# Kernel optimization log

Measured on AMD Instinct MI355X. Metric: run time of the kernel, lower is better.

The kernel has to match this reference:

```python
import jax, jax.numpy as jnp
import numpy as np

# Model dims (match init_kwargs)
D_MODEL = 1024
D_INNER = 2048
D_STATE = 16
D_CONV = 4
DT_RANK = 64
H = 8                      # num_heads
P = D_INNER // H           # head_dim = 256
DT_MIN, DT_MAX = 1e-4, 1.0
BATCH, SEQ = 2, 4096
TOTAL_OUT = 2 * D_INNER + DT_RANK + 2 * H * D_STATE  # 4416 (no gated delta)
EPS = 1e-6


def _xavier(k, shape):
    fan_out, fan_in = shape
    return jax.random.normal(k, shape, jnp.float32) * np.sqrt(2.0 / (fan_in + fan_out))


def setup_inputs() -> dict:
    key = jax.random.key(0)
    ks = jax.random.split(key, 8)
    x = jax.random.normal(ks[0], (BATCH, SEQ, D_MODEL), jnp.float32)
    W_in = _xavier(ks[1], (TOTAL_OUT, D_MODEL))          # in_proj (no bias)
    W_dt = _xavier(ks[2], (H, DT_RANK))                  # dt_proj (no bias)
    conv_w = jax.random.normal(ks[3], (D_INNER, D_CONV), jnp.float32) * 0.1
    conv_b = jnp.zeros((D_INNER,), jnp.float32)
    # A_log init: log(1..d_state) per head
    A_log = jnp.broadcast_to(jnp.log(jnp.arange(1, D_STATE + 1, dtype=jnp.float32)), (H, D_STATE))
    Dskip = jnp.ones((H, P), jnp.float32)
    # dt_bias = inverse_softplus(dt), dt log-uniform in [dt_min, dt_max]
    dt0 = jnp.exp(jax.random.uniform(ks[4], (H,), jnp.float32)
                  * (np.log(DT_MAX) - np.log(DT_MIN)) + np.log(DT_MIN))
    dt_bias = dt0 + jnp.log(-jnp.expm1(-dt0))
    norm_w = jnp.ones((D_INNER,), jnp.float32)
    W_out = _xavier(ks[5], (D_MODEL, D_INNER))
    W_res = _xavier(ks[6], (D_INNER, D_MODEL))           # residual_proj (d_model != d_inner)
    return dict(x=x, W_in=W_in, W_dt=W_dt, conv_w=conv_w, conv_b=conv_b,
                A_log=A_log, Dskip=Dskip, dt_bias=dt_bias, norm_w=norm_w,
                W_out=W_out, W_res=W_res)


def _causal_dwconv(u, w, b):
    # u: (B,L,C) -> causal depthwise conv along L. w: (C,K), b: (C,)
    lhs = u.transpose(0, 2, 1)               # (B,C,L)
    rhs = w[:, None, :]                      # (C,1,K)
    out = jax.lax.conv_general_dilated(
        lhs, rhs, window_strides=(1,), padding=[(D_CONV - 1, 0)],
        dimension_numbers=('NCH', 'OIH', 'NCH'), feature_group_count=D_INNER)
    return (out + b[None, :, None]).transpose(0, 2, 1)


def reference(x, W_in, W_dt, conv_w, conv_b, A_log, Dskip, dt_bias, norm_w, W_out, W_res):
    Bsz, L, _ = x.shape
    p = x @ W_in.T                                            # (B,L,TOTAL_OUT)
    splits = np.cumsum([D_INNER, D_INNER, DT_RANK, H * D_STATE]).tolist()
    z, u, dt_h, Bf, Cf = jnp.split(p, splits, axis=-1)
    Bp = Bf.reshape(Bsz, L, H, D_STATE)
    Cp = Cf.reshape(Bsz, L, H, D_STATE)
    u = _causal_dwconv(u, conv_w, conv_b)                     # (B,L,D_INNER)
    # dt_prep: softplus(dt_raw + bias) clamped to [dt_min, dt_max]
    dt = jnp.clip(jax.nn.softplus(dt_h @ W_dt.T + dt_bias), DT_MIN, DT_MAX)  # (B,L,H)
    A = -jnp.exp(A_log)                                       # (H,N)
    uh = u.reshape(Bsz, L, H, P)

    def step(h, inp):
        u_t, dt_t, B_t, C_t = inp                             # (B,H,P),(B,H),(B,H,N),(B,H,N)
        dA = jnp.exp(dt_t[..., None] * A)                     # (B,H,N)
        h = h * dA[:, :, None, :] + (dt_t[:, :, None, None] * u_t[..., None]) * B_t[:, :, None, :]
        y_t = jnp.einsum('bhpn,bhn->bhp', h, C_t)
        return h, y_t

    h0 = jnp.zeros((Bsz, H, P, D_STATE), x.dtype)
    xs = (uh.transpose(1, 0, 2, 3), dt.transpose(1, 0, 2),
          Bp.transpose(1, 0, 2, 3), Cp.transpose(1, 0, 2, 3))
    _, ys = jax.lax.scan(step, h0, xs)                        # (L,B,H,P)
    y = ys.transpose(1, 0, 2, 3) + Dskip[None, None] * uh     # skip connection
    y = y.reshape(Bsz, L, D_INNER)

    residual_inner = x @ W_res.T                              # residual_proj
    # fused_out: g = RMSNorm(y * silu(z) + residual) * weight
    g = y * jax.nn.silu(z) + residual_inner
    g = g * jax.lax.rsqrt(jnp.mean(g * g, axis=-1, keepdims=True) + EPS) * norm_w
    return g @ W_out.T
```

## Files before the change

kernel.cpp:

```cpp
#include <hip/hip_runtime.h>
#include <hip/hip_bf16.h>
#include <math.h>

#define DMODEL  1024
#define DINNER  2048
#define DSTATE  16
#define DCONV   4
#define DTRANK  64
#define NH      8
#define PH      256
#define TOTOUT  4416
#define NPAD    4608
#define NTOT    6656
#define MB_ROWS 4096
#define LC      64
#define NCB     (MB_ROWS/LC)

typedef __attribute__((ext_vector_type(8))) short bf16x8;
typedef __attribute__((ext_vector_type(4))) float f32x4;

__device__ inline unsigned cvt2bf(float lo, float hi) {
    unsigned r;
    asm("v_cvt_pk_bf16_f32 %0, %1, %2" : "=v"(r) : "v"(lo), "v"(hi));
    return r;
}
__device__ inline ushort f2bf(float v) { return (ushort)(cvt2bf(v, v) & 0xffffu); }
__device__ inline float bf2f(ushort u) {
    union { unsigned u; float f; } w; w.u = (unsigned)u << 16; return w.f;
}
__device__ inline void gload16(const ushort* g, ushort* l) {
    __builtin_amdgcn_global_load_lds((const __attribute__((address_space(1))) unsigned*)(const void*)g,
                                     (__attribute__((address_space(3))) unsigned*)(void*)l, 16, 0, 0);
}

__global__ __launch_bounds__(256) void cvt_bf(const float* __restrict__ s,
                                              ushort* __restrict__ d) {
    size_t i = ((size_t)blockIdx.x * 256 + threadIdx.x) * 8;
    float4 v0 = *(const float4*)(s + i);
    float4 v1 = *(const float4*)(s + i + 4);
    uint4 o;
    o.x = cvt2bf(v0.x, v0.y); o.y = cvt2bf(v0.z, v0.w);
    o.z = cvt2bf(v1.x, v1.y); o.w = cvt2bf(v1.z, v1.w);
    *(uint4*)(d + i) = o;
}

__global__ __launch_bounds__(256) void cvt_weights(const float* __restrict__ W_in,
                                                   const float* __restrict__ W_res,
                                                   const float* __restrict__ W_out,
                                                   ushort* __restrict__ dst) {
    const size_t E0 = (size_t)TOTOUT * DMODEL;
    const size_t E1 = (size_t)NPAD * DMODEL;
    const size_t E2 = (size_t)NTOT * DMODEL;
    size_t i = ((size_t)blockIdx.x * 256 + threadIdx.x) * 8;
    float4 v0, v1;
    if (i < E1) {
        if (i < E0) { v0 = *(const float4*)(W_in + i); v1 = *(const float4*)(W_in + i + 4); }
        else { v0 = make_float4(0.f,0.f,0.f,0.f); v1 = v0; }
    } else if (i < E2) {
        size_t o = i - E1; v0 = *(const float4*)(W_res + o); v1 = *(const float4*)(W_res + o + 4);
    } else {
        size_t o = i - E2; v0 = *(const float4*)(W_out + o); v1 = *(const float4*)(W_out + o + 4);
    }
    uint4 o;
    o.x = cvt2bf(v0.x, v0.y); o.y = cvt2bf(v0.z, v0.w);
    o.z = cvt2bf(v1.x, v1.y); o.w = cvt2bf(v1.z, v1.w);
    *(uint4*)(dst + i) = o;
}

__global__ __launch_bounds__(512) void gemm_fused(const ushort* __restrict__ A,
                                                  const ushort* __restrict__ W,
                                                  ushort* __restrict__ Zb,
                                                  ushort* __restrict__ Ub,
                                                  float* __restrict__ DBCp,
                                                  ushort* __restrict__ RESb,
                                                  int ntx, int K) {
    __shared__ __align__(16) ushort L[3 * 12288];
    const int nwg  = gridDim.x;
    const int orig = blockIdx.x;
    const int swz  = (orig & 7) * (nwg >> 3) + (orig >> 3);
    const int bx = swz % ntx, by = swz / ntx;
    const int row0 = by * 256, col0 = bx * 128;

    const int t    = threadIdx.x;
    const int lane = t & 63, w = t >> 6;
    const int wr   = w >> 1, wc = w & 1;
    const int l15  = lane & 15, l4 = lane >> 4;

    const int r0g = t >> 2, s0g = t & 3;
    const int r1g = r0g + 128;
    const int rr0 = r0g ^ ((r0g >> 3) & 1), cc0 = s0g ^ ((r0g >> 1) & 3);
    const int rr1 = r1g ^ ((r1g >> 3) & 1), cc1 = s0g ^ ((r1g >> 1) & 3);
    const ushort* sA0 = A + (size_t)(row0 + rr0) * K + cc0 * 8;
    const ushort* sA1 = A + (size_t)(row0 + rr1) * K + cc1 * 8;
    const ushort* sB0 = W + (size_t)(col0 + rr0) * K + cc0 * 8;

    int offA[4], offB[4];
    #pragma unroll
    for (int mi = 0; mi < 4; mi++) {
        int rq = wr * 64 + mi * 16 + l15;
        offA[mi] = (rq * 32 + l4 * 8) ^ (((rq >> 1) & 7) << 3);
    }
    #pragma unroll
    for (int ni = 0; ni < 4; ni++) {
        int rq = wc * 64 + ni * 16 + l15;
        offB[ni] = 8192 + ((rq * 32 + l4 * 8) ^ (((rq >> 1) & 7) << 3));
    }

    f32x4 acc[4][4];
    #pragma unroll
    for (int i = 0; i < 4; i++)
        #pragma unroll
        for (int j = 0; j < 4; j++)
            acc[i][j] = (f32x4){0.f, 0.f, 0.f, 0.f};

    const int KT = K >> 5;
    gload16(sA0,      &L[t * 8]);
    gload16(sA1,      &L[4096 + t * 8]);
    gload16(sB0,      &L[8192 + t * 8]);
    gload16(sA0 + 32, &L[12288 + t * 8]);
    gload16(sA1 + 32, &L[12288 + 4096 + t * 8]);
    gload16(sB0 + 32, &L[12288 + 8192 + t * 8]);
    asm volatile("s_waitcnt vmcnt(3)" ::: "memory");
    __builtin_amdgcn_sched_barrier(0);
    __builtin_amdgcn_s_barrier();
    __builtin_amdgcn_sched_barrier(0);

    for (int kt = 0; kt < KT; ++kt) {
        const bool pre = (kt + 2) < KT;
        if (pre) {
            ushort* bp2 = &L[((kt + 2) % 3) * 12288];
            const int ko = (kt + 2) << 5;
            gload16(sA0 + ko, bp2 + t * 8);
            gload16(sA1 + ko, bp2 + 4096 + t * 8);
            gload16(sB0 + ko, bp2 + 8192 + t * 8);
        }
        const ushort* bp = &L[(kt % 3) * 12288];
        bf16x8 af[4], bw[4];
        #pragma unroll
        for (int mi = 0; mi < 4; mi++) af[mi] = *(const bf16x8*)(bp + offA[mi]);
        #pragma unroll
        for (int ni = 0; ni < 4; ni++) bw[ni] = *(const bf16x8*)(bp + offB[ni]);
        __builtin_amdgcn_s_setprio(1);
        #pragma unroll
        for (int mi = 0; mi < 4; mi++)
            #pragma unroll
            for (int ni = 0; ni < 4; ni++)
                acc[mi][ni] = __builtin_amdgcn_mfma_f32_16x16x32_bf16(af[mi], bw[ni], acc[mi][ni], 0, 0, 0);
        __builtin_amdgcn_s_setprio(0);
        if (pre) { asm volatile("s_waitcnt vmcnt(3)" ::: "memory"); }
        else     { asm volatile("s_waitcnt vmcnt(0)" ::: "memory"); }
        __builtin_amdgcn_sched_barrier(0);
        __builtin_amdgcn_s_barrier();
        __builtin_amdgcn_sched_barrier(0);
    }

    #pragma unroll
    for (int mi = 0; mi < 4; mi++) {
        #pragma unroll
        for (int ni = 0; ni < 4; ni++) {
            #pragma unroll
            for (int rr = 0; rr < 4; rr++) {
                const int row = row0 + wr * 64 + mi * 16 + l4 * 4 + rr;
                const int col = col0 + wc * 64 + ni * 16 + l15;
                const float v = acc[mi][ni][rr];
                if (col0 < DINNER) {
                    Zb[(size_t)row * DINNER + col] = f2bf(v);
                } else if (col0 < 2 * DINNER) {
                    Ub[(size_t)row * DINNER + (col - DINNER)] = f2bf(v);
                } else if (col0 < NPAD) {
                    if (col < TOTOUT)
                        DBCp[(size_t)row * 320 + (col - 2 * DINNER)] = v;
                } else {
                    RESb[(size_t)row * DINNER + (col - NPAD)] = f2bf(v);
                }
            }
        }
    }
}

__global__ __launch_bounds__(256) void gemm_out128(const ushort* __restrict__ A,
                                                   const ushort* __restrict__ W,
                                                   float* __restrict__ C0,
                                                   int ntx, int K, int ldc) {
    __shared__ __align__(16) ushort L[3 * 8192];
    const int nwg  = gridDim.x;
    const int orig = blockIdx.x;
    const int swz  = (orig & 7) * (nwg >> 3) + (orig >> 3);
    const int bx = swz % ntx, by = swz / ntx;
    const int row0 = by * 128, col0 = bx * 128;

    const int t    = threadIdx.x;
    const int lane = t & 63, w = t >> 6;
    const int wr   = w >> 1, wc = w & 1;
    const int l15  = lane & 15, l4 = lane >> 4;

    const int r0g = t >> 2, s0g = t & 3;
    const int r1g = r0g + 64;
    const int rr0 = r0g ^ ((r0g >> 3) & 1), cc0 = s0g ^ ((r0g >> 1) & 3);
    const int rr1 = r1g ^ ((r1g >> 3) & 1), cc1 = s0g ^ ((r1g >> 1) & 3);
    const ushort* sA0 = A + (size_t)(row0 + rr0) * K + cc0 * 8;
    const ushort* sA1 = A + (size_t)(row0 + rr1) * K + cc1 * 8;
    const ushort* sB0 = W + (size_t)(col0 + rr0) * K + cc0 * 8;
    const ushort* sB1 = W + (size_t)(col0 + rr1) * K + cc1 * 8;

    int offA[4], offB[4];
    #pragma unroll
    for (int mi = 0; mi < 4; mi++) {
        int rq = wr * 64 + mi * 16 + l15;
        offA[mi] = (rq * 32 + l4 * 8) ^ (((rq >> 1) & 7) << 3);
    }
    #pragma unroll
    for (int ni = 0; ni < 4; ni++) {
        int rq = wc * 64 + ni * 16 + l15;
        offB[ni] = 4096 + ((rq * 32 + l4 * 8) ^ (((rq >> 1) & 7) << 3));
    }

    f32x4 acc[4][4];
    #pragma unroll
    for (int i = 0; i < 4; i++)
        #pragma unroll
        for (int j = 0; j < 4; j++)
            acc[i][j] = (f32x4){0.f, 0.f, 0.f, 0.f};

    const int KT = K >> 5;
    gload16(sA0,      &L[t * 8]);
    gload16(sA1,      &L[2048 + t * 8]);
    gload16(sB0,      &L[4096 + t * 8]);
    gload16(sB1,      &L[6144 + t * 8]);
    gload16(sA0 + 32, &L[8192 + t * 8]);
    gload16(sA1 + 32, &L[8192 + 2048 + t * 8]);
    gload16(sB0 + 32, &L[8192 + 4096 + t * 8]);
    gload16(sB1 + 32, &L[8192 + 6144 + t * 8]);
    asm volatile("s_waitcnt vmcnt(4)" ::: "memory");
    __builtin_amdgcn_sched_barrier(0);
    __builtin_amdgcn_s_barrier();
    __builtin_amdgcn_sched_barrier(0);

    for (int kt = 0; kt < KT; ++kt) {
        const bool pre = (kt + 2) < KT;
        if (pre) {
            ushort* bp2 = &L[((kt + 2) % 3) * 8192];
            const int ko = (kt + 2) << 5;
            gload16(sA0 + ko, bp2 + t * 8);
            gload16(sA1 + ko, bp2 + 2048 + t * 8);
            gload16(sB0 + ko, bp2 + 4096 + t * 8);
            gload16(sB1 + ko, bp2 + 6144 + t * 8);
        }
        const ushort* bp = &L[(kt % 3) * 8192];
        bf16x8 af[4], bw[4];
        #pragma unroll
        for (int mi = 0; mi < 4; mi++) af[mi] = *(const bf16x8*)(bp + offA[mi]);
        #pragma unroll
        for (int ni = 0; ni < 4; ni++) bw[ni] = *(const bf16x8*)(bp + offB[ni]);
        __builtin_amdgcn_s_setprio(1);
        #pragma unroll
        for (int mi = 0; mi < 4; mi++)
            #pragma unroll
            for (int ni = 0; ni < 4; ni++)
                acc[mi][ni] = __builtin_amdgcn_mfma_f32_16x16x32_bf16(af[mi], bw[ni], acc[mi][ni], 0, 0, 0);
        __builtin_amdgcn_s_setprio(0);
        if (pre) { asm volatile("s_waitcnt vmcnt(4)" ::: "memory"); }
        else     { asm volatile("s_waitcnt vmcnt(0)" ::: "memory"); }
        __builtin_amdgcn_sched_barrier(0);
        __builtin_amdgcn_s_barrier();
        __builtin_amdgcn_sched_barrier(0);
    }

    #pragma unroll
    for (int mi = 0; mi < 4; mi++)
        #pragma unroll
        for (int ni = 0; ni < 4; ni++)
            #pragma unroll
            for (int rr = 0; rr < 4; rr++) {
                const int row = row0 + wr * 64 + mi * 16 + l4 * 4 + rr;
                const int col = col0 + wc * 64 + ni * 16 + l15;
                C0[(size_t)row * ldc + col] = acc[mi][ni][rr];
            }
}

__global__ __launch_bounds__(256) void dt_kernel(const float* __restrict__ DBC,
                                                 const float* __restrict__ W_dt,
                                                 const float* __restrict__ dt_bias,
                                                 const float* __restrict__ A_log,
                                                 float* __restrict__ dt,
                                                 float* __restrict__ dA) {
    int idx = blockIdx.x * blockDim.x + threadIdx.x;
    int h = idx % NH;
    int tr = idx / NH;
    const float* row = DBC + (size_t)tr * 320;
    float acc = dt_bias[h];
    #pragma unroll
    for (int r = 0; r < DTRANK; r++) acc = fmaf(row[r], W_dt[h * DTRANK + r], acc);
    float sp = acc > 20.f ? acc : log1pf(expf(acc));
    sp = fminf(fmaxf(sp, 1e-4f), 1.0f);
    dt[idx] = sp;
    #pragma unroll
    for (int n = 0; n < DSTATE; n++)
        dA[(size_t)idx * DSTATE + n] = expf(sp * (-expf(A_log[h * DSTATE + n])));
}

__global__ __launch_bounds__(256) void scan_local(const ushort* __restrict__ Ub,
                                                  const float* __restrict__ DBC,
                                                  const float* __restrict__ dt_,
                                                  const float* __restrict__ dA_,
                                                  const float* __restrict__ cw,
                                                  const float* __restrict__ cb,
                                                  float* __restrict__ hloc,
                                                  float* __restrict__ Pc) {
    const int c = blockIdx.x, h = blockIdx.y;
    const int pidx = threadIdx.x;
    const int ch = h * PH + pidx;
    const int t0 = c * LC;
    __shared__ float sdA[LC][DSTATE];
    __shared__ float sdB[LC][DSTATE];
    const int st = pidx >> 4, sn = pidx & 15;
    #pragma unroll
    for (int j = 0; j < 4; j++) {
        int tt = st + j * 16;
        size_t trow = (size_t)(t0 + tt);
        float dv = dt_[trow * NH + h];
        sdA[tt][sn] = dA_[(trow * NH + h) * DSTATE + sn];
        sdB[tt][sn] = dv * DBC[trow * 320 + 64 + h * DSTATE + sn];
    }
    const float w0 = cw[ch * 4], w1 = cw[ch * 4 + 1], w2 = cw[ch * 4 + 2], w3 = cw[ch * 4 + 3];
    const float bia = cb[ch];
    const int bs = (c / NCB) * MB_ROWS;
    float um3 = (t0 - 3 >= bs) ? bf2f(Ub[(size_t)(t0 - 3) * DINNER + ch]) : 0.f;
    float um2 = (t0 - 2 >= bs) ? bf2f(Ub[(size_t)(t0 - 2) * DINNER + ch]) : 0.f;
    float um1 = (t0 - 1 >= bs) ? bf2f(Ub[(size_t)(t0 - 1) * DINNER + ch]) : 0.f;
    __syncthreads();

    float hst[DSTATE] = {};
    for (int t = 0; t < LC; t++) {
        float u0 = bf2f(Ub[(size_t)(t0 + t) * DINNER + ch]);
        float up = fmaf(w3, u0, fmaf(w2, um1, fmaf(w1, um2, fmaf(w0, um3, bia))));
        um3 = um2; um2 = um1; um1 = u0;
        #pragma unroll
        for (int n = 0; n < DSTATE; n++)
            hst[n] = fmaf(hst[n], sdA[t][n], up * sdB[t][n]);
    }
    float* hl = hloc + (((size_t)c * NH + h) * PH + pidx) * DSTATE;
    #pragma unroll
    for (int n = 0; n < DSTATE; n++) hl[n] = hst[n];

    if (pidx < DSTATE) {
        float pr = 1.f;
        for (int t = 0; t < LC; t++) pr *= sdA[t][pidx];
        Pc[((size_t)c * NH + h) * DSTATE + pidx] = pr;
    }
}

__global__ __launch_bounds__(256) void scan_carry(const float* __restrict__ hloc,
                                                  const float* __restrict__ Pc,
                                                  float* __restrict__ Hent) {
    int g = blockIdx.x * 256 + threadIdx.x;
    int b = g >> 15;
    int r = g & 32767;
    int h = r >> 12;
    int inner = r & 4095;
    int n = r & 15;
    float carry = 0.f;
    for (int i = 0; i < NCB; i++) {
        int c = b * NCB + i;
        size_t idx = ((size_t)c * NH + h) * (PH * DSTATE) + inner;
        Hent[idx] = carry;
        carry = fmaf(Pc[((size_t)c * NH + h) * DSTATE + n], carry, hloc[idx]);
    }
}

__global__ __launch_bounds__(256) void scan_out(const ushort* __restrict__ Zb,
                                                const ushort* __restrict__ Ub,
                                                const ushort* __restrict__ RESb,
                                                ushort* __restrict__ Yb,
                                                const float* __restrict__ DBC,
                                                const float* __restrict__ dt_,
                                                const float* __restrict__ dA_,
                                                const float* __restrict__ cw,
                                                const float* __restrict__ cb,
                                                const float* __restrict__ Dskip,
                                                const float* __restrict__ Hent) {
    const int c = blockIdx.x, h = blockIdx.y;
    const int pidx = threadIdx.x;
    const int ch = h * PH + pidx;
    const int t0 = c * LC;
    __shared__ float sdA[LC][DSTATE];
    __shared__ float sdB[LC][DSTATE];
    __shared__ float sC [LC][DSTATE];
    const int st = pidx >> 4, sn = pidx & 15;
    #pragma unroll
    for (int j = 0; j < 4; j++) {
        int tt = st + j * 16;
        size_t trow = (size_t)(t0 + tt);
        float dv = dt_[trow * NH + h];
        sdA[tt][sn] = dA_[(trow * NH + h) * DSTATE + sn];
        sdB[tt][sn] = dv * DBC[trow * 320 + 64 + h * DSTATE + sn];
        sC [tt][sn] =      DBC[trow * 320 + 192 + h * DSTATE + sn];
    }
    const float w0 = cw[ch * 4], w1 = cw[ch * 4 + 1], w2 = cw[ch * 4 + 2], w3 = cw[ch * 4 + 3];
    const float bia = cb[ch];
    const int bs = (c / NCB) * MB_ROWS;
    float um3 = (t0 - 3 >= bs) ? bf2f(Ub[(size_t)(t0 - 3) * DINNER + ch]) : 0.f;
    float um2 = (t0 - 2 >= bs) ? bf2f(Ub[(size_t)(t0 - 2) * DINNER + ch]) : 0.f;
    float um1 = (t0 - 1 >= bs) ? bf2f(Ub[(size_t)(t0 - 1) * DINNER + ch]) : 0.f;
    const float dsk = Dskip[ch];
    float hst[DSTATE];
    const float* he = Hent + (((size_t)c * NH + h) * PH + pidx) * DSTATE;
    #pragma unroll
    for (int n = 0; n < DSTATE; n++) hst[n] = he[n];
    __syncthreads();

    for (int t = 0; t < LC; t++) {
        size_t off = (size_t)(t0 + t) * DINNER + ch;
        float u0 = bf2f(Ub[off]);
        float up = fmaf(w3, u0, fmaf(w2, um1, fmaf(w1, um2, fmaf(w0, um3, bia))));
        um3 = um2; um2 = um1; um1 = u0;
        float a0 = 0.f, a1 = 0.f, a2 = 0.f, a3 = 0.f;
        #pragma unroll
        for (int n = 0; n < 4; n++) {
            hst[n +  0] = fmaf(hst[n +  0], sdA[t][n +  0], up * sdB[t][n +  0]);
            hst[n +  4] = fmaf(hst[n +  4], sdA[t][n +  4], up * sdB[t][n +  4]);
            hst[n +  8] = fmaf(hst[n +  8], sdA[t][n +  8], up * sdB[t][n +  8]);
            hst[n + 12] = fmaf(hst[n + 12], sdA[t][n + 12], up * sdB[t][n + 12]);
            a0 = fmaf(hst[n +  0], sC[t][n +  0], a0);
            a1 = fmaf(hst[n +  4], sC[t][n +  4], a1);
            a2 = fmaf(hst[n +  8], sC[t][n +  8], a2);
            a3 = fmaf(hst[n + 12], sC[t][n + 12], a3);
        }
        float yv = ((a0 + a1) + (a2 + a3)) + dsk * up;
        float zv = bf2f(Zb[off]);
        float sil = zv / (1.f + expf(-zv));
        Yb[off] = f2bf(fmaf(yv, sil, bf2f(RESb[off])));
    }
}

__global__ __launch_bounds__(256) void rmsnorm_bf(const ushort* __restrict__ Yb,
                                                  const float* __restrict__ norm_w,
                                                  ushort* __restrict__ Gb) {
    const int row = blockIdx.x;
    const ushort* r = Yb + (size_t)row * DINNER;
    const int c0 = threadIdx.x * 8;
    uint4 packed = *(const uint4*)(r + c0);
    float v[8];
    v[0] = bf2f((ushort)(packed.x & 0xffff)); v[1] = bf2f((ushort)(packed.x >> 16));
    v[2] = bf2f((ushort)(packed.y & 0xffff)); v[3] = bf2f((ushort)(packed.y >> 16));
    v[4] = bf2f((ushort)(packed.z & 0xffff)); v[5] = bf2f((ushort)(packed.z >> 16));
    v[6] = bf2f((ushort)(packed.w & 0xffff)); v[7] = bf2f((ushort)(packed.w >> 16));
    float ss = 0.f;
    #pragma unroll
    for (int i = 0; i < 8; i++) ss = fmaf(v[i], v[i], ss);
    #pragma unroll
    for (int off = 32; off > 0; off >>= 1) ss += __shfl_down(ss, off);
    __shared__ float red[4];
    if ((threadIdx.x & 63) == 0) red[threadIdx.x >> 6] = ss;
    __syncthreads();
    float tot = red[0] + red[1] + red[2] + red[3];
    float inv = rsqrtf(tot / (float)DINNER + 1e-6f);
    float4 w0 = *(const float4*)(norm_w + c0);
    float4 w1 = *(const float4*)(norm_w + c0 + 4);
    uint4 o;
    o.x = cvt2bf(v[0] * inv * w0.x, v[1] * inv * w0.y);
    o.y = cvt2bf(v[2] * inv * w0.z, v[3] * inv * w0.w);
    o.z = cvt2bf(v[4] * inv * w1.x, v[5] * inv * w1.y);
    o.w = cvt2bf(v[6] * inv * w1.z, v[7] * inv * w1.w);
    *(uint4*)(Gb + (size_t)row * DINNER + c0) = o;
}

struct Lay {
    float *DBC, *DT, *DA, *PC, *HLOC, *HENT;
    ushort *YB, *ZB, *UB, *RESB, *XBF, *WB;
    size_t total;
};
static Lay mk_layout(char* base, int Mr) {
    size_t o = 0;
    auto take = [&](size_t bytes) { char* p = base + o; o = (o + bytes + 255) & ~(size_t)255; return p; };
    Lay l;
    l.YB   = (ushort*)take((size_t)Mr * 2048 * 2);
    l.DBC  = (float*) take((size_t)Mr * 320 * 4);
    l.DT   = (float*) take((size_t)Mr * 8 * 4);
    l.DA   = (float*) take((size_t)Mr * 128 * 4);
    l.PC   = (float*) take((size_t)(Mr / 64) * NH * DSTATE * 4);
    l.HLOC = (float*) take((size_t)Mr * 512 * 4);
    l.HENT = (float*) take((size_t)Mr * 512 * 4);
    l.ZB   = (ushort*)take((size_t)Mr * 2048 * 2);
    l.UB   = (ushort*)take((size_t)Mr * 2048 * 2);
    l.RESB = (ushort*)take((size_t)Mr * 2048 * 2);
    l.XBF  = (ushort*)take((size_t)8192 * 1024 * 2);
    l.WB   = (ushort*)take(((size_t)NTOT * 1024 + (size_t)1024 * 2048) * 2);
    l.total = o;
    return l;
}

extern "C" void kernel_launch(void* const* d_in, const int* in_sizes, int n_in,
                              void* d_out, int out_size, void* d_ws, size_t ws_size,
                              hipStream_t stream) {
    const float* x       = (const float*)d_in[0];
    const float* W_in    = (const float*)d_in[1];
    const float* W_dt    = (const float*)d_in[2];
    const float* conv_w  = (const float*)d_in[3];
    const float* conv_b  = (const float*)d_in[4];
    const float* A_log   = (const float*)d_in[5];
    const float* Dskip   = (const float*)d_in[6];
    const float* dt_bias = (const float*)d_in[7];
    const float* norm_w  = (const float*)d_in[8];
    const float* W_out   = (const float*)d_in[9];
    const float* W_res   = (const float*)d_in[10];
    float* out = (float*)d_out;

    Lay probe = mk_layout(nullptr, 2 * MB_ROWS);
    const bool fat = ws_size >= probe.total;
    const int Mr = fat ? 2 * MB_ROWS : MB_ROWS;
    const int npass = fat ? 1 : 2;
    const int nbc = fat ? 2 : 1;
    Lay l = mk_layout((char*)d_ws, Mr);

    ushort* wcat = l.WB;
    ushort* wotb = wcat + (size_t)NTOT * 1024;
    ushort* Gb   = l.ZB;

    cvt_weights<<<((NTOT * 1024 + 2048 * 1024) / 8) / 256, 256, 0, stream>>>(W_in, W_res, W_out, l.WB);
    cvt_bf<<<(2 * MB_ROWS * DMODEL / 8) / 256, 256, 0, stream>>>(x, l.XBF);

    for (int b = 0; b < npass; b++) {
        const ushort* xb = l.XBF + (size_t)b * MB_ROWS * DMODEL;
        float* outb = out + (size_t)b * MB_ROWS * DMODEL;

        gemm_fused<<<52 * (Mr / 256), 512, 0, stream>>>(xb, wcat, l.ZB, l.UB, l.DBC, l.RESB, 52, DMODEL);
        dt_kernel<<<(Mr * NH) / 256, 256, 0, stream>>>(l.DBC, W_dt, dt_bias, A_log, l.DT, l.DA);
        scan_local<<<dim3(Mr / LC, NH), 256, 0, stream>>>(l.UB, l.DBC, l.DT, l.DA, conv_w, conv_b, l.HLOC, l.PC);
        scan_carry<<<nbc * 128, 256, 0, stream>>>(l.HLOC, l.PC, l.HENT);
        scan_out<<<dim3(Mr / LC, NH), 256, 0, stream>>>(l.ZB, l.UB, l.RESB, l.YB, l.DBC, l.DT, l.DA,
                                                        conv_w, conv_b, Dskip, l.HENT);
        rmsnorm_bf<<<Mr, 256, 0, stream>>>(l.YB, norm_w, Gb);
        gemm_out128<<<8 * (Mr / 128), 256, 0, stream>>>(Gb, wotb, outb, 8, DINNER, DMODEL);
    }
}
```

Measured before the change: 305.7 us.

## Fuse dt computation into scan kernels, merge conversions, shrink fused GEMM padding

The weight and input bf16 conversions become a single launch. The concatenated weight is reordered (z, u, res, then dt/B/C padded to 6528 rows), so the fused GEMM needs 51 column tiles instead of 52. The separate dt_kernel and its DT/DA buffers are removed: each scan_local and scan_out block now computes softplus(dt) for its 64 rows in shared memory and evaluates exp(dt*A) inline. This saves kernel launches, global round trips and some padded GEMM work, but the dt projection is now computed twice. An extra barrier is also placed in the GEMM main loop between the LDS reads and the MFMAs.

```diff
diff --git a/kernel.cpp b/kernel.cpp
--- a/kernel.cpp
+++ b/kernel.cpp
@@ -10,8 +10,7 @@
 #define NH      8
 #define PH      256
 #define TOTOUT  4416
-#define NPAD    4608
-#define NTOT    6656
+#define NTOT2   6528
 #define MB_ROWS 4096
 #define LC      64
 #define NCB     (MB_ROWS/LC)
@@ -33,46 +32,47 @@
                                      (__attribute__((address_space(3))) unsigned*)(void*)l, 16, 0, 0);
 }
 
-__global__ __launch_bounds__(256) void cvt_bf(const float* __restrict__ s,
-                                              ushort* __restrict__ d) {
+__global__ __launch_bounds__(256) void cvt_all(const float* __restrict__ W_in,
+                                               const float* __restrict__ W_res,
+                                               const float* __restrict__ W_out,
+                                               const float* __restrict__ x,
+                                               ushort* __restrict__ WB,
+                                               ushort* __restrict__ XBF) {
+    const size_t E_WCAT = (size_t)NTOT2 * DMODEL;
+    const size_t E_WOUT = E_WCAT + (size_t)DMODEL * DINNER;
     size_t i = ((size_t)blockIdx.x * 256 + threadIdx.x) * 8;
-    float4 v0 = *(const float4*)(s + i);
-    float4 v1 = *(const float4*)(s + i + 4);
+    const float* src;
+    ushort* dst;
+    bool zero = false;
+    if (i < E_WCAT) {
+        size_t r = i >> 10, c = i & 1023;
+        if (r < 4096)       src = W_in + (r << 10) + c;
+        else if (r < 6144)  src = W_res + ((r - 4096) << 10) + c;
+        else if (r < 6464)  src = W_in + ((r - 2048) << 10) + c;
+        else { src = W_in; zero = true; }
+        dst = WB + i;
+    } else if (i < E_WOUT) {
+        src = W_out + (i - E_WCAT);
+        dst = WB + i;
+    } else {
+        src = x + (i - E_WOUT);
+        dst = XBF + (i - E_WOUT);
+    }
+    float4 v0, v1;
+    if (zero) { v0 = make_float4(0.f, 0.f, 0.f, 0.f); v1 = v0; }
+    else { v0 = *(const float4*)src; v1 = *(const float4*)(src + 4); }
     uint4 o;
     o.x = cvt2bf(v0.x, v0.y); o.y = cvt2bf(v0.z, v0.w);
     o.z = cvt2bf(v1.x, v1.y); o.w = cvt2bf(v1.z, v1.w);
-    *(uint4*)(d + i) = o;
-}
-
-__global__ __launch_bounds__(256) void cvt_weights(const float* __restrict__ W_in,
-                                                   const float* __restrict__ W_res,
-                                                   const float* __restrict__ W_out,
-                                                   ushort* __restrict__ dst) {
-    const size_t E0 = (size_t)TOTOUT * DMODEL;
-    const size_t E1 = (size_t)NPAD * DMODEL;
-    const size_t E2 = (size_t)NTOT * DMODEL;
-    size_t i = ((size_t)blockIdx.x * 256 + threadIdx.x) * 8;
-    float4 v0, v1;
-    if (i < E1) {
-        if (i < E0) { v0 = *(const float4*)(W_in + i); v1 = *(const float4*)(W_in + i + 4); }
-        else { v0 = make_float4(0.f,0.f,0.f,0.f); v1 = v0; }
-    } else if (i < E2) {
-        size_t o = i - E1; v0 = *(const float4*)(W_res + o); v1 = *(const float4*)(W_res + o + 4);
-    } else {
-        size_t o = i - E2; v0 = *(const float4*)(W_out + o); v1 = *(const float4*)(W_out + o + 4);
-    }
-    uint4 o;
-    o.x = cvt2bf(v0.x, v0.y); o.y = cvt2bf(v0.z, v0.w);
-    o.z = cvt2bf(v1.x, v1.y); o.w = cvt2bf(v1.z, v1.w);
-    *(uint4*)(dst + i) = o;
+    *(uint4*)dst = o;
 }
 
 __global__ __launch_bounds__(512) void gemm_fused(const ushort* __restrict__ A,
                                                   const ushort* __restrict__ W,
                                                   ushort* __restrict__ Zb,
                                                   ushort* __restrict__ Ub,
+                                                  ushort* __restrict__ RESb,
                                                   float* __restrict__ DBCp,
-                                                  ushort* __restrict__ RESb,
                                                   int ntx, int K) {
     __shared__ __align__(16) ushort L[3 * 12288];
     const int nwg  = gridDim.x;
@@ -140,6 +140,9 @@
         for (int mi = 0; mi < 4; mi++) af[mi] = *(const bf16x8*)(bp + offA[mi]);
         #pragma unroll
         for (int ni = 0; ni < 4; ni++) bw[ni] = *(const bf16x8*)(bp + offB[ni]);
+        __builtin_amdgcn_sched_barrier(0);
+        __builtin_amdgcn_s_barrier();
+        __builtin_amdgcn_sched_barrier(0);
         __builtin_amdgcn_s_setprio(1);
         #pragma unroll
         for (int mi = 0; mi < 4; mi++)
@@ -167,11 +170,11 @@
                     Zb[(size_t)row * DINNER + col] = f2bf(v);
                 } else if (col0 < 2 * DINNER) {
                     Ub[(size_t)row * DINNER + (col - DINNER)] = f2bf(v);
-                } else if (col0 < NPAD) {
-                    if (col < TOTOUT)
-                        DBCp[(size_t)row * 320 + (col - 2 * DINNER)] = v;
+                } else if (col0 < 3 * DINNER) {
+                    RESb[(size_t)row * DINNER + (col - 2 * DINNER)] = f2bf(v);
                 } else {
-                    RESb[(size_t)row * DINNER + (col - NPAD)] = f2bf(v);
+                    if (col < 3 * DINNER + 320)
+                        DBCp[(size_t)row * 320 + (col - 3 * DINNER)] = v;
                 }
             }
         }
@@ -278,31 +281,11 @@
             }
 }
 
-__global__ __launch_bounds__(256) void dt_kernel(const float* __restrict__ DBC,
-                                                 const float* __restrict__ W_dt,
-                                                 const float* __restrict__ dt_bias,
-                                                 const float* __restrict__ A_log,
-                                                 float* __restrict__ dt,
-                                                 float* __restrict__ dA) {
-    int idx = blockIdx.x * blockDim.x + threadIdx.x;
-    int h = idx % NH;
-    int tr = idx / NH;
-    const float* row = DBC + (size_t)tr * 320;
-    float acc = dt_bias[h];
-    #pragma unroll
-    for (int r = 0; r < DTRANK; r++) acc = fmaf(row[r], W_dt[h * DTRANK + r], acc);
-    float sp = acc > 20.f ? acc : log1pf(expf(acc));
-    sp = fminf(fmaxf(sp, 1e-4f), 1.0f);
-    dt[idx] = sp;
-    #pragma unroll
-    for (int n = 0; n < DSTATE; n++)
-        dA[(size_t)idx * DSTATE + n] = expf(sp * (-expf(A_log[h * DSTATE + n])));
-}
-
 __global__ __launch_bounds__(256) void scan_local(const ushort* __restrict__ Ub,
                                                   const float* __restrict__ DBC,
-                                                  const float* __restrict__ dt_,
-                                                  const float* __restrict__ dA_,
+                                                  const float* __restrict__ W_dt,
+                                                  const float* __restrict__ dt_bias,
+                                                  const float* __restrict__ A_log,
                                                   const float* __restrict__ cw,
                                                   const float* __restrict__ cb,
                                                   float* __restrict__ hloc,
@@ -311,16 +294,19 @@
     const int pidx = threadIdx.x;
     const int ch = h * PH + pidx;
     const int t0 = c * LC;
+    __shared__ float sdt[LC];
     __shared__ float sdA[LC][DSTATE];
     __shared__ float sdB[LC][DSTATE];
     const int st = pidx >> 4, sn = pidx & 15;
-    #pragma unroll
-    for (int j = 0; j < 4; j++) {
-        int tt = st + j * 16;
-        size_t trow = (size_t)(t0 + tt);
-        float dv = dt_[trow * NH + h];
-        sdA[tt][sn] = dA_[(trow * NH + h) * DSTATE + sn];
-        sdB[tt][sn] = dv * DBC[trow * 320 + 64 + h * DSTATE + sn];
+
+    if (pidx < LC) {
+        const float* row = DBC + (size_t)(t0 + pidx) * 320;
+        const float* wd = W_dt + h * DTRANK;
+        float acc = dt_bias[h];
+        #pragma unroll 16
+        for (int r2 = 0; r2 < DTRANK; r2++) acc = fmaf(row[r2], wd[r2], acc);
+        float sp = acc > 20.f ? acc : log1pf(expf(acc));
+        sdt[pidx] = fminf(fmaxf(sp, 1e-4f), 1.0f);
     }
     const float w0 = cw[ch * 4], w1 = cw[ch * 4 + 1], w2 = cw[ch * 4 + 2], w3 = cw[ch * 4 + 3];
     const float bia = cb[ch];
@@ -328,6 +314,19 @@
     float um3 = (t0 - 3 >= bs) ? bf2f(Ub[(size_t)(t0 - 3) * DINNER + ch]) : 0.f;
     float um2 = (t0 - 2 >= bs) ? bf2f(Ub[(size_t)(t0 - 2) * DINNER + ch]) : 0.f;
     float um1 = (t0 - 1 >= bs) ? bf2f(Ub[(size_t)(t0 - 1) * DINNER + ch]) : 0.f;
+    __syncthreads();
+
+    {
+        const float nA = -expf(A_log[h * DSTATE + sn]);
+        #pragma unroll
+        for (int j = 0; j < 4; j++) {
+            int tt = st + j * 16;
+            size_t trow = (size_t)(t0 + tt);
+            float dv = sdt[tt];
+            sdA[tt][sn] = expf(dv * nA);
+            sdB[tt][sn] = dv * DBC[trow * 320 + 64 + h * DSTATE + sn];
+        }
+    }
     __syncthreads();
 
     float hst[DSTATE] = {};
@@ -373,8 +372,9 @@
                                                 const ushort* __restrict__ RESb,
                                                 ushort* __restrict__ Yb,
                                                 const float* __restrict__ DBC,
-                                                const float* __restrict__ dt_,
-                                                const float* __restrict__ dA_,
+                                                const float* __restrict__ W_dt,
+                                                const float* __restrict__ dt_bias,
+                                                const float* __restrict__ A_log,
                                                 const float* __restrict__ cw,
                                                 const float* __restrict__ cb,
                                                 const float* __restrict__ Dskip,
@@ -383,18 +383,20 @@
     const int pidx = threadIdx.x;
     const int ch = h * PH + pidx;
     const int t0 = c * LC;
+    __shared__ float sdt[LC];
     __shared__ float sdA[LC][DSTATE];
     __shared__ float sdB[LC][DSTATE];
     __shared__ float sC [LC][DSTATE];
     const int st = pidx >> 4, sn = pidx & 15;
-    #pragma unroll
-    for (int j = 0; j < 4; j++) {
-        int tt = st + j * 16;
-        size_t trow = (size_t)(t0 + tt);
-        float dv = dt_[trow * NH + h];
-        sdA[tt][sn] = dA_[(trow * NH + h) * DSTATE + sn];
-        sdB[tt][sn] = dv * DBC[trow * 320 + 64 + h * DSTATE + sn];
-        sC [tt][sn] =      DBC[trow * 320 + 192 + h * DSTATE + sn];
+
+    if (pidx < LC) {
+        const float* row = DBC + (size_t)(t0 + pidx) * 320;
+        const float* wd = W_dt + h * DTRANK;
+        float acc = dt_bias[h];
+        #pragma unroll 16
+        for (int r2 = 0; r2 < DTRANK; r2++) acc = fmaf(row[r2], wd[r2], acc);
+        float sp = acc > 20.f ? acc : log1pf(expf(acc));
+        sdt[pidx] = fminf(fmaxf(sp, 1e-4f), 1.0f);
     }
     const float w0 = cw[ch * 4], w1 = cw[ch * 4 + 1], w2 = cw[ch * 4 + 2], w3 = cw[ch * 4 + 3];
     const float bia = cb[ch];
@@ -402,6 +404,20 @@
     float um3 = (t0 - 3 >= bs) ? bf2f(Ub[(size_t)(t0 - 3) * DINNER + ch]) : 0.f;
     float um2 = (t0 - 2 >= bs) ? bf2f(Ub[(size_t)(t0 - 2) * DINNER + ch]) : 0.f;
     float um1 = (t0 - 1 >= bs) ? bf2f(Ub[(size_t)(t0 - 1) * DINNER + ch]) : 0.f;
+    __syncthreads();
+
+    {
+        const float nA = -expf(A_log[h * DSTATE + sn]);
+        #pragma unroll
+        for (int j = 0; j < 4; j++) {
+            int tt = st + j * 16;
+            size_t trow = (size_t)(t0 + tt);
+            float dv = sdt[tt];
+            sdA[tt][sn] = expf(dv * nA);
+            sdB[tt][sn] = dv * DBC[trow * 320 + 64 + h * DSTATE + sn];
+            sC [tt][sn] =      DBC[trow * 320 + 192 + h * DSTATE + sn];
+        }
+    }
     const float dsk = Dskip[ch];
     float hst[DSTATE];
     const float* he = Hent + (((size_t)c * NH + h) * PH + pidx) * DSTATE;
@@ -466,7 +482,7 @@
 }
 
 struct Lay {
-    float *DBC, *DT, *DA, *PC, *HLOC, *HENT;
+    float *DBC, *PC, *HLOC, *HENT;
     ushort *YB, *ZB, *UB, *RESB, *XBF, *WB;
     size_t total;
 };
@@ -476,8 +492,6 @@
     Lay l;
     l.YB   = (ushort*)take((size_t)Mr * 2048 * 2);
     l.DBC  = (float*) take((size_t)Mr * 320 * 4);
-    l.DT   = (float*) take((size_t)Mr * 8 * 4);
-    l.DA   = (float*) take((size_t)Mr * 128 * 4);
     l.PC   = (float*) take((size_t)(Mr / 64) * NH * DSTATE * 4);
     l.HLOC = (float*) take((size_t)Mr * 512 * 4);
     l.HENT = (float*) take((size_t)Mr * 512 * 4);
@@ -485,7 +499,7 @@
     l.UB   = (ushort*)take((size_t)Mr * 2048 * 2);
     l.RESB = (ushort*)take((size_t)Mr * 2048 * 2);
     l.XBF  = (ushort*)take((size_t)8192 * 1024 * 2);
-    l.WB   = (ushort*)take(((size_t)NTOT * 1024 + (size_t)1024 * 2048) * 2);
+    l.WB   = (ushort*)take(((size_t)NTOT2 * 1024 + (size_t)1024 * 2048) * 2);
     l.total = o;
     return l;
 }
@@ -514,21 +528,24 @@
     Lay l = mk_layout((char*)d_ws, Mr);
 
     ushort* wcat = l.WB;
-    ushort* wotb = wcat + (size_t)NTOT * 1024;
+    ushort* wotb = wcat + (size_t)NTOT2 * 1024;
     ushort* Gb   = l.ZB;
 
-    cvt_weights<<<((NTOT * 1024 + 2048 * 1024) / 8) / 256, 256, 0, stream>>>(W_in, W_res, W_out, l.WB);
-    cvt_bf<<<(2 * MB_ROWS * DMODEL / 8) / 256, 256, 0, stream>>>(x, l.XBF);
+    {
+        const size_t total_gran = ((size_t)NTOT2 * 1024 + (size_t)1024 * 2048 + (size_t)8192 * 1024) / 8;
+        cvt_all<<<(int)(total_gran / 256), 256, 0, stream>>>(W_in, W_res, W_out, x, l.WB, l.XBF);
+    }
 
     for (int b = 0; b < npass; b++) {
         const ushort* xb = l.XBF + (size_t)b * MB_ROWS * DMODEL;
         float* outb = out + (size_t)b * MB_ROWS * DMODEL;
 
-        gemm_fused<<<52 * (Mr / 256), 512, 0, stream>>>(xb, wcat, l.ZB, l.UB, l.DBC, l.RESB, 52, DMODEL);
-        dt_kernel<<<(Mr * NH) / 256, 256, 0, stream>>>(l.DBC, W_dt, dt_bias, A_log, l.DT, l.DA);
-        scan_local<<<dim3(Mr / LC, NH), 256, 0, stream>>>(l.UB, l.DBC, l.DT, l.DA, conv_w, conv_b, l.HLOC, l.PC);
+        gemm_fused<<<51 * (Mr / 256), 512, 0, stream>>>(xb, wcat, l.ZB, l.UB, l.RESB, l.DBC, 51, DMODEL);
+        scan_local<<<dim3(Mr / LC, NH), 256, 0, stream>>>(l.UB, l.DBC, W_dt, dt_bias, A_log,
+                                                          conv_w, conv_b, l.HLOC, l.PC);
         scan_carry<<<nbc * 128, 256, 0, stream>>>(l.HLOC, l.PC, l.HENT);
-        scan_out<<<dim3(Mr / LC, NH), 256, 0, stream>>>(l.ZB, l.UB, l.RESB, l.YB, l.DBC, l.DT, l.DA,
+        scan_out<<<dim3(Mr / LC, NH), 256, 0, stream>>>(l.ZB, l.UB, l.RESB, l.YB, l.DBC,
+                                                        W_dt, dt_bias, A_log,
                                                         conv_w, conv_b, Dskip, l.HENT);
         rmsnorm_bf<<<Mr, 256, 0, stream>>>(l.YB, norm_w, Gb);
         gemm_out128<<<8 * (Mr / 128), 256, 0, stream>>>(Gb, wotb, outb, 8, DINNER, DMODEL);
```

After: 300.6 us. Within noise of the previous version (-1.7%).
